# Kernel tuning notes

Measured on AMD Instinct MI355X. Metric: run time of the kernel, lower is better.

Reference implementation:

```python
import jax, jax.numpy as jnp
import numpy as np

NUM_HEADS = 16


def setup_inputs() -> dict:
    key = jax.random.key(0)
    ks = jax.random.split(key, 8)
    B, T, E = 2, 2048, 1024
    hd = E // NUM_HEADS
    return {
        "x": jax.random.normal(ks[0], (B, T, E), jnp.float32),
        "attn_mask_re": jax.random.normal(ks[1], (B, 1, T, hd // 2), jnp.float32),
        "attn_mask_im": jax.random.normal(ks[2], (B, 1, T, hd // 2), jnp.float32),
        "pad_mask": jax.random.normal(ks[3], (B, 1, 1, T), jnp.float32),
        "qkv_w": jax.random.normal(ks[4], (3 * E, E), jnp.float32) * 0.02,
        "qkv_b": jax.random.normal(ks[5], (3 * E,), jnp.float32) * 0.02,
        "o_w": jax.random.normal(ks[6], (E, E), jnp.float32) * 0.02,
        "o_b": jax.random.normal(ks[7], (E,), jnp.float32) * 0.02,
    }


def reference(x, attn_mask_re, attn_mask_im, pad_mask, qkv_w, qkv_b, o_w, o_b):
    B, T, E = x.shape
    H = NUM_HEADS
    hd = E // H
    scale = 1.0 / jnp.sqrt(jnp.asarray(hd, x.dtype))
    # fused QKV projection
    qkv = x @ qkv_w.T + qkv_b            # [B,T,3E]
    q, k, v = jnp.split(qkv, 3, axis=-1)
    q = q.reshape(B, T, H, hd).transpose(0, 2, 1, 3)          # [B,H,T,hd]
    v = v.reshape(B, T, H, hd).transpose(0, 2, 1, 3)          # [B,H,T,hd]
    # rotary on k via complex multiply: k viewed as [B,H,T,hd/2] complex
    kc = k.reshape(B, T, H, hd // 2, 2).transpose(0, 2, 1, 3, 4)  # [B,H,T,hd/2,2]
    kr, ki = kc[..., 0], kc[..., 1]
    mr, mi = attn_mask_re, attn_mask_im   # [B,1,T,hd/2] broadcast over heads
    rr = kr * mr - ki * mi
    ri = kr * mi + ki * mr
    k_rot = jnp.stack([rr, ri], axis=-1).reshape(B, H, T, hd)  # [B,H,T,hd]
    # attention scores [B,H,T,T]
    a = jnp.einsum("bhqd,bhkd->bhqk", q, k_rot) * scale
    a = a + pad_mask
    a = jax.nn.softmax(a, axis=-1)
    # (eval mode: attention dropout is a no-op)
    o = jnp.einsum("bhqk,bhkd->bhqd", a, v)                    # [B,H,T,hd]
    o = o.transpose(0, 2, 1, 3).reshape(B, T, E)
    o = o @ o_w.T + o_b
    a_avg = a.sum(axis=1) / H                                  # [B,T,T]
    return o, a_avg
```

## Files before the change

kernel.cpp:

```cpp
#include <hip/hip_runtime.h>
#include <math.h>

#define TSEQ 2048
#define EMB  1024
#define NH   16
#define HD   64
#define NB   2
#define L2E  1.4426950408889634f

#if defined(__has_builtin)
#if __has_builtin(__builtin_amdgcn_exp2f)
#define EXP2(x) __builtin_amdgcn_exp2f(x)
#else
#define EXP2(x) exp2f(x)
#endif
#else
#define EXP2(x) exp2f(x)
#endif

typedef unsigned short u16;
typedef unsigned int   u32;
typedef __attribute__((ext_vector_type(8))) short short8v;
typedef __attribute__((ext_vector_type(4))) float f32x4;

#define MFMA16(a,b,c) __builtin_amdgcn_mfma_f32_16x16x32_bf16(a,b,c,0,0,0)

__device__ inline u32 f2bf(float x) {
    u32 u = __float_as_uint(x);
    return (u + 0x7fffu + ((u >> 16) & 1u)) >> 16;
}
__device__ inline float bf2f(u32 b) { return __uint_as_float(b << 16); }
__device__ inline void split4(float x0, float x1, float x2, float x3,
                              u32& hw0, u32& hw1, u32& lw0, u32& lw1) {
    u32 h0 = f2bf(x0), h1 = f2bf(x1), h2 = f2bf(x2), h3 = f2bf(x3);
    u32 l0 = f2bf(x0 - bf2f(h0)), l1 = f2bf(x1 - bf2f(h1));
    u32 l2 = f2bf(x2 - bf2f(h2)), l3 = f2bf(x3 - bf2f(h3));
    hw0 = h0 | (h1 << 16); hw1 = h2 | (h3 << 16);
    lw0 = l0 | (l1 << 16); lw1 = l2 | (l3 << 16);
}

__global__ __launch_bounds__(256) void conv_split_kernel(
    const float* __restrict__ in, u16* __restrict__ hi, u16* __restrict__ lo)
{
    const size_t i = (size_t)blockIdx.x * 256 + threadIdx.x;
    float4 v = ((const float4*)in)[i];
    u32 hw0, hw1, lw0, lw1;
    split4(v.x, v.y, v.z, v.w, hw0, hw1, lw0, lw1);
    *(uint2*)(hi + i * 4) = make_uint2(hw0, hw1);
    *(uint2*)(lo + i * 4) = make_uint2(lw0, lw1);
}

#define MM_CORE(Ah_, Al_, Bh_, Bl_, Kdim)                                      \
    __shared__ __align__(16) u16 sAh[128][40], sAl[128][40];                   \
    __shared__ __align__(16) u16 sBh[128][40], sBl[128][40];                   \
    const int tid = threadIdx.x;                                               \
    const int lane = tid & 63, w = tid >> 6;                                   \
    const int lc = lane & 15, lg = lane >> 4;                                  \
    const int wr = w >> 1, wc = w & 1;                                         \
    const int i0 = blockIdx.x * 128, j0 = blockIdx.y * 128;                    \
    const int srow = tid >> 1, shalf = (tid & 1) << 4;                         \
    const u16* pAh = Ah_ + (size_t)(i0 + srow) * Kdim + shalf;                 \
    const u16* pAl = Al_ + (size_t)(i0 + srow) * Kdim + shalf;                 \
    const u16* pBh = Bh_ + (size_t)(j0 + srow) * Kdim + shalf;                 \
    const u16* pBl = Bl_ + (size_t)(j0 + srow) * Kdim + shalf;                 \
    f32x4 acc[4][4];                                                           \
    _Pragma("unroll")                                                          \
    for (int rs = 0; rs < 4; ++rs)                                             \
        _Pragma("unroll")                                                      \
        for (int cs = 0; cs < 4; ++cs) acc[rs][cs] = (f32x4){0.f,0.f,0.f,0.f};\
    for (int k0 = 0; k0 < Kdim; k0 += 32) {                                    \
        short8v va0 = *(const short8v*)(pAh + k0);                             \
        short8v va1 = *(const short8v*)(pAh + k0 + 8);                         \
        short8v vb0 = *(const short8v*)(pAl + k0);                             \
        short8v vb1 = *(const short8v*)(pAl + k0 + 8);                         \
        short8v vc0 = *(const short8v*)(pBh + k0);                             \
        short8v vc1 = *(const short8v*)(pBh + k0 + 8);                         \
        short8v vd0 = *(const short8v*)(pBl + k0);                             \
        short8v vd1 = *(const short8v*)(pBl + k0 + 8);                         \
        *(short8v*)&sAh[srow][shalf]     = va0;                                \
        *(short8v*)&sAh[srow][shalf + 8] = va1;                                \
        *(short8v*)&sAl[srow][shalf]     = vb0;                                \
        *(short8v*)&sAl[srow][shalf + 8] = vb1;                                \
        *(short8v*)&sBh[srow][shalf]     = vc0;                                \
        *(short8v*)&sBh[srow][shalf + 8] = vc1;                                \
        *(short8v*)&sBl[srow][shalf]     = vd0;                                \
        *(short8v*)&sBl[srow][shalf + 8] = vd1;                                \
        __syncthreads();                                                       \
        short8v fah[4], fal[4], fbh[4], fbl[4];                                \
        _Pragma("unroll")                                                      \
        for (int rs = 0; rs < 4; ++rs) {                                       \
            fah[rs] = *(const short8v*)&sAh[wr*64 + rs*16 + lc][lg*8];         \
            fal[rs] = *(const short8v*)&sAl[wr*64 + rs*16 + lc][lg*8];         \
        }                                                                      \
        _Pragma("unroll")                                                      \
        for (int cs = 0; cs < 4; ++cs) {                                       \
            fbh[cs] = *(const short8v*)&sBh[wc*64 + cs*16 + lc][lg*8];         \
            fbl[cs] = *(const short8v*)&sBl[wc*64 + cs*16 + lc][lg*8];         \
        }                                                                      \
        _Pragma("unroll")                                                      \
        for (int rs = 0; rs < 4; ++rs)                                         \
            _Pragma("unroll")                                                  \
            for (int cs = 0; cs < 4; ++cs) {                                   \
                acc[rs][cs] = MFMA16(fah[rs], fbh[cs], acc[rs][cs]);           \
                acc[rs][cs] = MFMA16(fah[rs], fbl[cs], acc[rs][cs]);           \
                acc[rs][cs] = MFMA16(fal[rs], fbh[cs], acc[rs][cs]);           \
            }                                                                  \
        __syncthreads();                                                       \
    }

__global__ __launch_bounds__(256) void mm_qkv_kernel(
    const u16* __restrict__ Ah, const u16* __restrict__ Al,
    const u16* __restrict__ Bh, const u16* __restrict__ Bl,
    const float* __restrict__ bias,
    u16* __restrict__ qhi, u16* __restrict__ qlo,
    u16* __restrict__ khi, u16* __restrict__ klo,
    u16* __restrict__ vthi, u16* __restrict__ vtlo)
{
    MM_CORE(Ah, Al, Bh, Bl, EMB)

    const int which = j0 >> 10;
    #pragma unroll
    for (int cs = 0; cs < 4; ++cs) {
        const int j = j0 + wc*64 + cs*16 + lc;
        const float bj = bias[j];
        const int e = j & (EMB - 1);
        const int hh = e >> 6, d = e & (HD - 1);
        #pragma unroll
        for (int rs = 0; rs < 4; ++rs) {
            #pragma unroll
            for (int r = 0; r < 4; ++r) {
                const int i = i0 + wr*64 + rs*16 + lg*4 + r;
                const int b = i >> 11, t = i & (TSEQ - 1);
                float val = acc[rs][cs][r] + bj;
                if (which == 0) val *= 0.125f;
                const u32 vh = f2bf(val);
                const u32 vl = f2bf(val - bf2f(vh));
                if (which == 2) {
                    const size_t ix = ((size_t)(b * NH + hh) * HD + d) * TSEQ + t;
                    vthi[ix] = (u16)vh; vtlo[ix] = (u16)vl;
                } else {
                    const size_t ix = ((size_t)(b * NH + hh) * TSEQ + t) * HD + d;
                    if (which == 0) { qhi[ix] = (u16)vh; qlo[ix] = (u16)vl; }
                    else            { khi[ix] = (u16)vh; klo[ix] = (u16)vl; }
                }
            }
        }
    }
}

__global__ __launch_bounds__(256) void mm_out_kernel(
    const u16* __restrict__ Ah, const u16* __restrict__ Al,
    const u16* __restrict__ Bh, const u16* __restrict__ Bl,
    const float* __restrict__ bias, float* __restrict__ C)
{
    MM_CORE(Ah, Al, Bh, Bl, EMB)

    #pragma unroll
    for (int cs = 0; cs < 4; ++cs) {
        const int j = j0 + wc*64 + cs*16 + lc;
        const float bj = bias[j];
        #pragma unroll
        for (int rs = 0; rs < 4; ++rs) {
            #pragma unroll
            for (int r = 0; r < 4; ++r) {
                const int i = i0 + wr*64 + rs*16 + lg*4 + r;
                C[(size_t)i * EMB + j] = acc[rs][cs][r] + bj;
            }
        }
    }
}

__global__ __launch_bounds__(256) void rotary_k_kernel(
    u16* __restrict__ khi, u16* __restrict__ klo,
    const float* __restrict__ mre, const float* __restrict__ mim)
{
    const int idx = blockIdx.x * 256 + threadIdx.x;
    const int d2 = idx & 31;
    const int t  = (idx >> 5) & (TSEQ - 1);
    const int b  = idx >> 20;
    u32 h2 = *(u32*)(khi + ((size_t)idx << 1));
    u32 l2 = *(u32*)(klo + ((size_t)idx << 1));
    float kr = bf2f(h2 & 0xffff) + bf2f(l2 & 0xffff);
    float ki = bf2f(h2 >> 16) + bf2f(l2 >> 16);
    const int mix = (b * TSEQ + t) * 32 + d2;
    const float mr = mre[mix], mi = mim[mix];
    float rr = kr * mr - ki * mi;
    float ri = kr * mi + ki * mr;
    u32 hr = f2bf(rr), hx = f2bf(ri);
    u32 lr = f2bf(rr - bf2f(hr)), lx = f2bf(ri - bf2f(hx));
    *(u32*)(khi + ((size_t)idx << 1)) = hr | (hx << 16);
    *(u32*)(klo + ((size_t)idx << 1)) = lr | (lx << 16);
}

__global__ __launch_bounds__(128) void flash_attn_kernel(
    const u16* __restrict__ qhi_, const u16* __restrict__ qlo_,
    const u16* __restrict__ khi_, const u16* __restrict__ klo_,
    const u16* __restrict__ vthi_, const u16* __restrict__ vtlo_,
    const float* __restrict__ pad,
    u16* __restrict__ ohi, u16* __restrict__ olo,
    float* __restrict__ m_out, float* __restrict__ linv_out)
{
    __shared__ __align__(16) u16 Phi[2][32*40];
    __shared__ __align__(16) u16 Plo[2][32*40];

    const int tid  = threadIdx.x;
    const int lane = tid & 63;
    const int w    = tid >> 6;
    const int bh   = blockIdx.x >> 5;
    const int sub  = blockIdx.x & 31;
    const int b    = bh >> 4, h = bh & (NH - 1);
    const int qbase = sub * 64 + w * 32;
    const int lg = lane >> 4, lc = lane & 15;

    short8v qh[2][2], ql[2][2];
    #pragma unroll
    for (int qs = 0; qs < 2; ++qs) {
        const size_t qoff = ((size_t)bh * TSEQ + qbase + qs*16 + lc) * HD + lg*8;
        #pragma unroll
        for (int s = 0; s < 2; ++s) {
            qh[qs][s] = *(const short8v*)(qhi_ + qoff + s*32);
            ql[qs][s] = *(const short8v*)(qlo_ + qoff + s*32);
        }
    }

    f32x4 O[2][4];
    float mst[2][4], lst[2][4];
    #pragma unroll
    for (int qs = 0; qs < 2; ++qs) {
        #pragma unroll
        for (int db = 0; db < 4; ++db) O[qs][db] = (f32x4){0.f,0.f,0.f,0.f};
        #pragma unroll
        for (int r = 0; r < 4; ++r) { mst[qs][r] = -1e30f; lst[qs][r] = 0.f; }
    }

    u16* PHw = &Phi[w][0];
    u16* PLw = &Plo[w][0];
    const size_t kbase  = (size_t)bh * TSEQ * HD;
    const size_t vtbase = (size_t)bh * HD * TSEQ;

    for (int k0 = 0; k0 < TSEQ; k0 += 32) {
        f32x4 S[2][2];
        #pragma unroll
        for (int qs = 0; qs < 2; ++qs)
            #pragma unroll
            for (int kb2 = 0; kb2 < 2; ++kb2) S[qs][kb2] = (f32x4){0.f,0.f,0.f,0.f};
        #pragma unroll
        for (int kb2 = 0; kb2 < 2; ++kb2) {
            #pragma unroll
            for (int s = 0; s < 2; ++s) {
                const size_t ko = kbase + (size_t)(k0 + kb2*16 + lc) * HD + s*32 + lg*8;
                short8v kh = *(const short8v*)(khi_ + ko);
                short8v kl = *(const short8v*)(klo_ + ko);
                #pragma unroll
                for (int qs = 0; qs < 2; ++qs) {
                    S[qs][kb2] = MFMA16(qh[qs][s], kh, S[qs][kb2]);
                    S[qs][kb2] = MFMA16(qh[qs][s], kl, S[qs][kb2]);
                    S[qs][kb2] = MFMA16(ql[qs][s], kh, S[qs][kb2]);
                }
            }
        }

        const float pv0 = pad[b * TSEQ + k0 + lc];
        const float pv1 = pad[b * TSEQ + k0 + 16 + lc];

        #pragma unroll
        for (int qs = 0; qs < 2; ++qs) {
            #pragma unroll
            for (int r = 0; r < 4; ++r) {
                float s0 = S[qs][0][r] + pv0;
                float s1 = S[qs][1][r] + pv1;
                float t = fmaxf(s0, s1);
                t = fmaxf(t, __shfl_xor(t, 1));
                t = fmaxf(t, __shfl_xor(t, 2));
                t = fmaxf(t, __shfl_xor(t, 4));
                t = fmaxf(t, __shfl_xor(t, 8));
                const float mn = fmaxf(mst[qs][r], t);
                const float cc = EXP2((mst[qs][r] - mn) * L2E);
                const float p0 = EXP2((s0 - mn) * L2E);
                const float p1 = EXP2((s1 - mn) * L2E);
                float ps = p0 + p1;
                ps += __shfl_xor(ps, 1);
                ps += __shfl_xor(ps, 2);
                ps += __shfl_xor(ps, 4);
                ps += __shfl_xor(ps, 8);
                lst[qs][r] = lst[qs][r] * cc + ps;
                mst[qs][r] = mn;
                const int row = qs*16 + lg*4 + r;
                const u32 h0 = f2bf(p0), h1 = f2bf(p1);
                PHw[row*40 + lc]      = (u16)h0;
                PHw[row*40 + 16 + lc] = (u16)h1;
                PLw[row*40 + lc]      = (u16)f2bf(p0 - bf2f(h0));
                PLw[row*40 + 16 + lc] = (u16)f2bf(p1 - bf2f(h1));
                #pragma unroll
                for (int db = 0; db < 4; ++db) O[qs][db][r] *= cc;
            }
        }

        short8v pfh[2], pfl[2];
        #pragma unroll
        for (int qs = 0; qs < 2; ++qs) {
            pfh[qs] = *(const short8v*)(PHw + (qs*16 + lc)*40 + lg*8);
            pfl[qs] = *(const short8v*)(PLw + (qs*16 + lc)*40 + lg*8);
        }

        #pragma unroll
        for (int db = 0; db < 4; ++db) {
            const size_t vo = vtbase + (size_t)(db*16 + lc) * TSEQ + k0 + lg*8;
            short8v vh = *(const short8v*)(vthi_ + vo);
            short8v vl = *(const short8v*)(vtlo_ + vo);
            #pragma unroll
            for (int qs = 0; qs < 2; ++qs) {
                O[qs][db] = MFMA16(pfh[qs], vh, O[qs][db]);
                O[qs][db] = MFMA16(pfh[qs], vl, O[qs][db]);
                O[qs][db] = MFMA16(pfl[qs], vh, O[qs][db]);
            }
        }
    }

    #pragma unroll
    for (int qs = 0; qs < 2; ++qs) {
        #pragma unroll
        for (int r = 0; r < 4; ++r) {
            const float inv = 1.f / lst[qs][r];
            const int trow = qbase + qs*16 + lg*4 + r;
            const size_t obase = ((size_t)(b * TSEQ + trow)) * EMB + h * HD;
            #pragma unroll
            for (int db = 0; db < 4; ++db) {
                const float val = O[qs][db][r] * inv;
                const u32 vh = f2bf(val);
                ohi[obase + db*16 + lc] = (u16)vh;
                olo[obase + db*16 + lc] = (u16)f2bf(val - bf2f(vh));
            }
            if (lc == 0) {
                m_out[bh * TSEQ + trow] = mst[qs][r];
                linv_out[bh * TSEQ + trow] = inv;
            }
        }
    }
}

__global__ __launch_bounds__(256) void attn_avg_kernel(
    const u16* __restrict__ qhi_, const u16* __restrict__ qlo_,
    const u16* __restrict__ khi_, const u16* __restrict__ klo_,
    const float* __restrict__ pad, const float* __restrict__ m_arr,
    const float* __restrict__ linv_arr, float* __restrict__ a_avg)
{
    const int tid  = threadIdx.x;
    const int lane = tid & 63;
    const int w    = tid >> 6;
    const int b  = blockIdx.z;
    const int q0 = blockIdx.y << 5;
    const int k0 = blockIdx.x << 7;
    const int lg = lane >> 4, lc = lane & 15;
    const int kw = k0 + w * 32;

    const float pv0 = pad[b * TSEQ + kw + lc];
    const float pv1 = pad[b * TSEQ + kw + 16 + lc];

    f32x4 acc[2][2];
    #pragma unroll
    for (int qs = 0; qs < 2; ++qs)
        #pragma unroll
        for (int kb2 = 0; kb2 < 2; ++kb2) acc[qs][kb2] = (f32x4){0.f,0.f,0.f,0.f};

    for (int h = 0; h < NH; ++h) {
        const size_t hb = (size_t)(b * NH + h) * TSEQ;
        short8v qh[2][2], ql[2][2];
        #pragma unroll
        for (int qs = 0; qs < 2; ++qs) {
            const size_t qoff = (hb + q0 + qs*16 + lc) * HD + lg*8;
            #pragma unroll
            for (int s = 0; s < 2; ++s) {
                qh[qs][s] = *(const short8v*)(qhi_ + qoff + s*32);
                ql[qs][s] = *(const short8v*)(qlo_ + qoff + s*32);
            }
        }
        f32x4 S[2][2];
        #pragma unroll
        for (int qs = 0; qs < 2; ++qs)
            #pragma unroll
            for (int kb2 = 0; kb2 < 2; ++kb2) S[qs][kb2] = (f32x4){0.f,0.f,0.f,0.f};
        #pragma unroll
        for (int kb2 = 0; kb2 < 2; ++kb2) {
            #pragma unroll
            for (int s = 0; s < 2; ++s) {
                const size_t ko = (hb + kw + kb2*16 + lc) * HD + s*32 + lg*8;
                short8v kh = *(const short8v*)(khi_ + ko);
                short8v kl = *(const short8v*)(klo_ + ko);
                #pragma unroll
                for (int qs = 0; qs < 2; ++qs) {
                    S[qs][kb2] = MFMA16(qh[qs][s], kh, S[qs][kb2]);
                    S[qs][kb2] = MFMA16(qh[qs][s], kl, S[qs][kb2]);
                    S[qs][kb2] = MFMA16(ql[qs][s], kh, S[qs][kb2]);
                }
            }
        }
        #pragma unroll
        for (int qs = 0; qs < 2; ++qs) {
            #pragma unroll
            for (int r = 0; r < 4; ++r) {
                const size_t rix = hb + q0 + qs*16 + lg*4 + r;
                const float mh = m_arr[rix];
                const float li = linv_arr[rix];
                acc[qs][0][r] += EXP2((S[qs][0][r] + pv0 - mh) * L2E) * li;
                acc[qs][1][r] += EXP2((S[qs][1][r] + pv1 - mh) * L2E) * li;
            }
        }
    }

    const float invH = 1.0f / (float)NH;
    #pragma unroll
    for (int qs = 0; qs < 2; ++qs) {
        #pragma unroll
        for (int r = 0; r < 4; ++r) {
            const int row = q0 + qs*16 + lg*4 + r;
            #pragma unroll
            for (int kb2 = 0; kb2 < 2; ++kb2)
                a_avg[((size_t)b * TSEQ + row) * TSEQ + kw + kb2*16 + lc] =
                    acc[qs][kb2][r] * invH;
        }
    }
}

extern "C" void kernel_launch(void* const* d_in, const int* in_sizes, int n_in,
                              void* d_out, int out_size, void* d_ws, size_t ws_size,
                              hipStream_t stream)
{
    const float* x    = (const float*)d_in[0];
    const float* mre  = (const float*)d_in[1];
    const float* mim  = (const float*)d_in[2];
    const float* pad  = (const float*)d_in[3];
    const float* qkvw = (const float*)d_in[4];
    const float* qkvb = (const float*)d_in[5];
    const float* ow   = (const float*)d_in[6];
    const float* ob   = (const float*)d_in[7];

    float* out_o = (float*)d_out;
    float* out_a = out_o + (size_t)NB * TSEQ * EMB;

    u16* ohi = (u16*)out_a;
    u16* olo = ohi + (size_t)NB * TSEQ * EMB;

    const size_t SZ = (size_t)NB * NH * TSEQ * HD;
    u16* qhi  = (u16*)d_ws;
    u16* qlo  = qhi  + SZ;
    u16* khi  = qlo  + SZ;
    u16* klo  = khi  + SZ;
    u16* vthi = klo  + SZ;
    u16* vtlo = vthi + SZ;
    float* marr = (float*)(vtlo + SZ);
    float* linv = marr + (size_t)NB * NH * TSEQ;
    u16* xhi  = (u16*)(linv + (size_t)NB * NH * TSEQ);
    u16* xlo  = xhi + SZ;
    u16* whi  = xlo + SZ;
    u16* wlo  = whi + (size_t)3 * EMB * EMB;
    u16* owhi = wlo + (size_t)3 * EMB * EMB;
    u16* owlo = owhi + (size_t)EMB * EMB;

    conv_split_kernel<<<4096, 256, 0, stream>>>(x, xhi, xlo);
    conv_split_kernel<<<3072, 256, 0, stream>>>(qkvw, whi, wlo);
    conv_split_kernel<<<1024, 256, 0, stream>>>(ow, owhi, owlo);

    mm_qkv_kernel<<<dim3(32, 24), 256, 0, stream>>>(
        xhi, xlo, whi, wlo, qkvb, qhi, qlo, khi, klo, vthi, vtlo);

    rotary_k_kernel<<<8192, 256, 0, stream>>>(khi, klo, mre, mim);

    flash_attn_kernel<<<1024, 128, 0, stream>>>(
        qhi, qlo, khi, klo, vthi, vtlo, pad, ohi, olo, marr, linv);

    mm_out_kernel<<<dim3(32, 8), 256, 0, stream>>>(
        ohi, olo, owhi, owlo, ob, out_o);

    attn_avg_kernel<<<dim3(16, 64, 2), 256, 0, stream>>>(
        qhi, qlo, khi, klo, pad, marr, linv, out_a);
}
```

Baseline: 796.1 us.

## Halve per-wave query rows in flash attention, double grid, MFMA row sums

Each wave of the flash attention kernel now handles 16 query rows instead of 32, and the grid doubles to 2048 blocks with a min-blocks launch bound of 4. This cuts register use and raises occupancy. The softmax row-sum shuffle reduction is replaced by MFMAs of the bf16 P tiles against a ones vector, and the V loads are issued before the softmax so their latency overlaps it. The cost is that each K and V tile is now loaded from global memory twice as many times overall, since fewer query rows share it, and the row sum now comes from the bf16 hi/lo split of P rather than the fp32 values.

```diff
diff --git a/kernel.cpp b/kernel.cpp
--- a/kernel.cpp
+++ b/kernel.cpp
@@ -192,7 +192,7 @@
     *(u32*)(klo + ((size_t)idx << 1)) = lr | (lx << 16);
 }
 
-__global__ __launch_bounds__(128) void flash_attn_kernel(
+__global__ __launch_bounds__(128, 4) void flash_attn_kernel(
     const u16* __restrict__ qhi_, const u16* __restrict__ qlo_,
     const u16* __restrict__ khi_, const u16* __restrict__ klo_,
     const u16* __restrict__ vthi_, const u16* __restrict__ vtlo_,
@@ -200,38 +200,36 @@
     u16* __restrict__ ohi, u16* __restrict__ olo,
     float* __restrict__ m_out, float* __restrict__ linv_out)
 {
-    __shared__ __align__(16) u16 Phi[2][32*40];
-    __shared__ __align__(16) u16 Plo[2][32*40];
+    __shared__ __align__(16) u16 Phi[2][16*40];
+    __shared__ __align__(16) u16 Plo[2][16*40];
 
     const int tid  = threadIdx.x;
     const int lane = tid & 63;
     const int w    = tid >> 6;
-    const int bh   = blockIdx.x >> 5;
-    const int sub  = blockIdx.x & 31;
+    const int bh   = blockIdx.x >> 6;
+    const int sub  = blockIdx.x & 63;
     const int b    = bh >> 4, h = bh & (NH - 1);
-    const int qbase = sub * 64 + w * 32;
+    const int qbase = sub * 32 + w * 16;
     const int lg = lane >> 4, lc = lane & 15;
 
-    short8v qh[2][2], ql[2][2];
-    #pragma unroll
-    for (int qs = 0; qs < 2; ++qs) {
-        const size_t qoff = ((size_t)bh * TSEQ + qbase + qs*16 + lc) * HD + lg*8;
-        #pragma unroll
-        for (int s = 0; s < 2; ++s) {
-            qh[qs][s] = *(const short8v*)(qhi_ + qoff + s*32);
-            ql[qs][s] = *(const short8v*)(qlo_ + qoff + s*32);
-        }
-    }
-
-    f32x4 O[2][4];
-    float mst[2][4], lst[2][4];
-    #pragma unroll
-    for (int qs = 0; qs < 2; ++qs) {
-        #pragma unroll
-        for (int db = 0; db < 4; ++db) O[qs][db] = (f32x4){0.f,0.f,0.f,0.f};
-        #pragma unroll
-        for (int r = 0; r < 4; ++r) { mst[qs][r] = -1e30f; lst[qs][r] = 0.f; }
-    }
+    short8v qh[2], ql[2];
+    {
+        const size_t qoff = ((size_t)bh * TSEQ + qbase + lc) * HD + lg*8;
+        qh[0] = *(const short8v*)(qhi_ + qoff);
+        qh[1] = *(const short8v*)(qhi_ + qoff + 32);
+        ql[0] = *(const short8v*)(qlo_ + qoff);
+        ql[1] = *(const short8v*)(qlo_ + qoff + 32);
+    }
+
+    f32x4 O[4];
+    float mst[4], lst[4];
+    #pragma unroll
+    for (int db = 0; db < 4; ++db) O[db] = (f32x4){0.f,0.f,0.f,0.f};
+    #pragma unroll
+    for (int r = 0; r < 4; ++r) { mst[r] = -1e30f; lst[r] = 0.f; }
+
+    const short oneb = (short)0x3F80;
+    const short8v ones = {oneb,oneb,oneb,oneb,oneb,oneb,oneb,oneb};
 
     u16* PHw = &Phi[w][0];
     u16* PLw = &Plo[w][0];
@@ -239,11 +237,9 @@
     const size_t vtbase = (size_t)bh * HD * TSEQ;
 
     for (int k0 = 0; k0 < TSEQ; k0 += 32) {
-        f32x4 S[2][2];
-        #pragma unroll
-        for (int qs = 0; qs < 2; ++qs)
-            #pragma unroll
-            for (int kb2 = 0; kb2 < 2; ++kb2) S[qs][kb2] = (f32x4){0.f,0.f,0.f,0.f};
+        f32x4 S[2];
+        S[0] = (f32x4){0.f,0.f,0.f,0.f};
+        S[1] = (f32x4){0.f,0.f,0.f,0.f};
         #pragma unroll
         for (int kb2 = 0; kb2 < 2; ++kb2) {
             #pragma unroll
@@ -251,90 +247,80 @@
                 const size_t ko = kbase + (size_t)(k0 + kb2*16 + lc) * HD + s*32 + lg*8;
                 short8v kh = *(const short8v*)(khi_ + ko);
                 short8v kl = *(const short8v*)(klo_ + ko);
-                #pragma unroll
-                for (int qs = 0; qs < 2; ++qs) {
-                    S[qs][kb2] = MFMA16(qh[qs][s], kh, S[qs][kb2]);
-                    S[qs][kb2] = MFMA16(qh[qs][s], kl, S[qs][kb2]);
-                    S[qs][kb2] = MFMA16(ql[qs][s], kh, S[qs][kb2]);
-                }
-            }
+                S[kb2] = MFMA16(qh[s], kh, S[kb2]);
+                S[kb2] = MFMA16(qh[s], kl, S[kb2]);
+                S[kb2] = MFMA16(ql[s], kh, S[kb2]);
+            }
+        }
+
+        short8v vh[4], vl[4];
+        #pragma unroll
+        for (int db = 0; db < 4; ++db) {
+            const size_t vo = vtbase + (size_t)(db*16 + lc) * TSEQ + k0 + lg*8;
+            vh[db] = *(const short8v*)(vthi_ + vo);
+            vl[db] = *(const short8v*)(vtlo_ + vo);
         }
 
         const float pv0 = pad[b * TSEQ + k0 + lc];
         const float pv1 = pad[b * TSEQ + k0 + 16 + lc];
 
-        #pragma unroll
-        for (int qs = 0; qs < 2; ++qs) {
-            #pragma unroll
-            for (int r = 0; r < 4; ++r) {
-                float s0 = S[qs][0][r] + pv0;
-                float s1 = S[qs][1][r] + pv1;
-                float t = fmaxf(s0, s1);
-                t = fmaxf(t, __shfl_xor(t, 1));
-                t = fmaxf(t, __shfl_xor(t, 2));
-                t = fmaxf(t, __shfl_xor(t, 4));
-                t = fmaxf(t, __shfl_xor(t, 8));
-                const float mn = fmaxf(mst[qs][r], t);
-                const float cc = EXP2((mst[qs][r] - mn) * L2E);
-                const float p0 = EXP2((s0 - mn) * L2E);
-                const float p1 = EXP2((s1 - mn) * L2E);
-                float ps = p0 + p1;
-                ps += __shfl_xor(ps, 1);
-                ps += __shfl_xor(ps, 2);
-                ps += __shfl_xor(ps, 4);
-                ps += __shfl_xor(ps, 8);
-                lst[qs][r] = lst[qs][r] * cc + ps;
-                mst[qs][r] = mn;
-                const int row = qs*16 + lg*4 + r;
-                const u32 h0 = f2bf(p0), h1 = f2bf(p1);
-                PHw[row*40 + lc]      = (u16)h0;
-                PHw[row*40 + 16 + lc] = (u16)h1;
-                PLw[row*40 + lc]      = (u16)f2bf(p0 - bf2f(h0));
-                PLw[row*40 + 16 + lc] = (u16)f2bf(p1 - bf2f(h1));
-                #pragma unroll
-                for (int db = 0; db < 4; ++db) O[qs][db][r] *= cc;
-            }
-        }
-
-        short8v pfh[2], pfl[2];
-        #pragma unroll
-        for (int qs = 0; qs < 2; ++qs) {
-            pfh[qs] = *(const short8v*)(PHw + (qs*16 + lc)*40 + lg*8);
-            pfl[qs] = *(const short8v*)(PLw + (qs*16 + lc)*40 + lg*8);
-        }
+        float cc_[4];
+        #pragma unroll
+        for (int r = 0; r < 4; ++r) {
+            float s0 = S[0][r] + pv0;
+            float s1 = S[1][r] + pv1;
+            float t = fmaxf(s0, s1);
+            t = fmaxf(t, __shfl_xor(t, 1));
+            t = fmaxf(t, __shfl_xor(t, 2));
+            t = fmaxf(t, __shfl_xor(t, 4));
+            t = fmaxf(t, __shfl_xor(t, 8));
+            const float mn = fmaxf(mst[r], t);
+            cc_[r] = EXP2((mst[r] - mn) * L2E);
+            mst[r] = mn;
+            const float p0 = EXP2((s0 - mn) * L2E);
+            const float p1 = EXP2((s1 - mn) * L2E);
+            const int row = lg*4 + r;
+            const u32 h0 = f2bf(p0), h1 = f2bf(p1);
+            PHw[row*40 + lc]      = (u16)h0;
+            PHw[row*40 + 16 + lc] = (u16)h1;
+            PLw[row*40 + lc]      = (u16)f2bf(p0 - bf2f(h0));
+            PLw[row*40 + 16 + lc] = (u16)f2bf(p1 - bf2f(h1));
+            #pragma unroll
+            for (int db = 0; db < 4; ++db) O[db][r] *= cc_[r];
+        }
+
+        short8v pfh = *(const short8v*)(PHw + lc*40 + lg*8);
+        short8v pfl = *(const short8v*)(PLw + lc*40 + lg*8);
+
+        f32x4 Ss = (f32x4){0.f,0.f,0.f,0.f};
+        Ss = MFMA16(pfh, ones, Ss);
+        Ss = MFMA16(pfl, ones, Ss);
+        #pragma unroll
+        for (int r = 0; r < 4; ++r) lst[r] = lst[r] * cc_[r] + Ss[r];
 
         #pragma unroll
         for (int db = 0; db < 4; ++db) {
-            const size_t vo = vtbase + (size_t)(db*16 + lc) * TSEQ + k0 + lg*8;
-            short8v vh = *(const short8v*)(vthi_ + vo);
-            short8v vl = *(const short8v*)(vtlo_ + vo);
-            #pragma unroll
-            for (int qs = 0; qs < 2; ++qs) {
-                O[qs][db] = MFMA16(pfh[qs], vh, O[qs][db]);
-                O[qs][db] = MFMA16(pfh[qs], vl, O[qs][db]);
-                O[qs][db] = MFMA16(pfl[qs], vh, O[qs][db]);
-            }
-        }
-    }
-
-    #pragma unroll
-    for (int qs = 0; qs < 2; ++qs) {
-        #pragma unroll
-        for (int r = 0; r < 4; ++r) {
-            const float inv = 1.f / lst[qs][r];
-            const int trow = qbase + qs*16 + lg*4 + r;
-            const size_t obase = ((size_t)(b * TSEQ + trow)) * EMB + h * HD;
-            #pragma unroll
-            for (int db = 0; db < 4; ++db) {
-                const float val = O[qs][db][r] * inv;
-                const u32 vh = f2bf(val);
-                ohi[obase + db*16 + lc] = (u16)vh;
-                olo[obase + db*16 + lc] = (u16)f2bf(val - bf2f(vh));
-            }
-            if (lc == 0) {
-                m_out[bh * TSEQ + trow] = mst[qs][r];
-                linv_out[bh * TSEQ + trow] = inv;
-            }
+            O[db] = MFMA16(pfh, vh[db], O[db]);
+            O[db] = MFMA16(pfh, vl[db], O[db]);
+            O[db] = MFMA16(pfl, vh[db], O[db]);
+        }
+    }
+
+    #pragma unroll
+    for (int r = 0; r < 4; ++r) {
+        const float inv = 1.f / lst[r];
+        const int trow = qbase + lg*4 + r;
+        const size_t obase = ((size_t)(b * TSEQ + trow)) * EMB + h * HD;
+        #pragma unroll
+        for (int db = 0; db < 4; ++db) {
+            const float val = O[db][r] * inv;
+            const u32 vhp = f2bf(val);
+            ohi[obase + db*16 + lc] = (u16)vhp;
+            olo[obase + db*16 + lc] = (u16)f2bf(val - bf2f(vhp));
+        }
+        if (lc == 0) {
+            m_out[bh * TSEQ + trow] = mst[r];
+            linv_out[bh * TSEQ + trow] = inv;
         }
     }
 }
@@ -466,7 +452,7 @@
 
     rotary_k_kernel<<<8192, 256, 0, stream>>>(khi, klo, mre, mim);
 
-    flash_attn_kernel<<<1024, 128, 0, stream>>>(
+    flash_attn_kernel<<<2048, 128, 0, stream>>>(
         qhi, qlo, khi, klo, vthi, vtlo, pad, ohi, olo, marr, linv);
 
     mm_out_kernel<<<dim3(32, 8), 256, 0, stream>>>(
```

After: 948.5 us. 1.19x slower.

## Remap blocks per XCD, prefetch V tiles, compute row sums via MFMA

Applied to the files above, without the earlier changes.

Both the flash attention and attention-average kernels now decode a linear block id so that consecutive blocks sharing the same (batch, head) or key tile land on the same XCD, which should raise L2 reuse of K/V. In flash attention, V fragments are loaded before the softmax so the load latency overlaps the exponentials. The per-row sum of probabilities now comes from an MFMA against a vector of ones instead of shuffle reductions. The MFMA row sum uses the bf16-split probabilities, so it carries a small rounding difference, and the extra live V registers may lower occupancy.

```diff
diff --git a/kernel.cpp b/kernel.cpp
--- a/kernel.cpp
+++ b/kernel.cpp
@@ -206,8 +206,11 @@
     const int tid  = threadIdx.x;
     const int lane = tid & 63;
     const int w    = tid >> 6;
-    const int bh   = blockIdx.x >> 5;
-    const int sub  = blockIdx.x & 31;
+    const int bid  = blockIdx.x;
+    const int xcd  = bid & 7;
+    const int local= bid >> 3;
+    const int bh   = xcd * 4 + (local >> 5);
+    const int sub  = local & 31;
     const int b    = bh >> 4, h = bh & (NH - 1);
     const int qbase = sub * 64 + w * 32;
     const int lg = lane >> 4, lc = lane & 15;
@@ -232,6 +235,9 @@
         #pragma unroll
         for (int r = 0; r < 4; ++r) { mst[qs][r] = -1e30f; lst[qs][r] = 0.f; }
     }
+
+    const short oneb = (short)0x3F80;
+    const short8v ones = {oneb,oneb,oneb,oneb,oneb,oneb,oneb,oneb};
 
     u16* PHw = &Phi[w][0];
     u16* PLw = &Plo[w][0];
@@ -260,9 +266,18 @@
             }
         }
 
+        short8v vh[4], vl[4];
+        #pragma unroll
+        for (int db = 0; db < 4; ++db) {
+            const size_t vo = vtbase + (size_t)(db*16 + lc) * TSEQ + k0 + lg*8;
+            vh[db] = *(const short8v*)(vthi_ + vo);
+            vl[db] = *(const short8v*)(vtlo_ + vo);
+        }
+
         const float pv0 = pad[b * TSEQ + k0 + lc];
         const float pv1 = pad[b * TSEQ + k0 + 16 + lc];
 
+        float cc_[2][4];
         #pragma unroll
         for (int qs = 0; qs < 2; ++qs) {
             #pragma unroll
@@ -275,16 +290,10 @@
                 t = fmaxf(t, __shfl_xor(t, 4));
                 t = fmaxf(t, __shfl_xor(t, 8));
                 const float mn = fmaxf(mst[qs][r], t);
-                const float cc = EXP2((mst[qs][r] - mn) * L2E);
+                cc_[qs][r] = EXP2((mst[qs][r] - mn) * L2E);
+                mst[qs][r] = mn;
                 const float p0 = EXP2((s0 - mn) * L2E);
                 const float p1 = EXP2((s1 - mn) * L2E);
-                float ps = p0 + p1;
-                ps += __shfl_xor(ps, 1);
-                ps += __shfl_xor(ps, 2);
-                ps += __shfl_xor(ps, 4);
-                ps += __shfl_xor(ps, 8);
-                lst[qs][r] = lst[qs][r] * cc + ps;
-                mst[qs][r] = mn;
                 const int row = qs*16 + lg*4 + r;
                 const u32 h0 = f2bf(p0), h1 = f2bf(p1);
                 PHw[row*40 + lc]      = (u16)h0;
@@ -292,7 +301,7 @@
                 PLw[row*40 + lc]      = (u16)f2bf(p0 - bf2f(h0));
                 PLw[row*40 + 16 + lc] = (u16)f2bf(p1 - bf2f(h1));
                 #pragma unroll
-                for (int db = 0; db < 4; ++db) O[qs][db][r] *= cc;
+                for (int db = 0; db < 4; ++db) O[qs][db][r] *= cc_[qs][r];
             }
         }
 
@@ -304,15 +313,21 @@
         }
 
         #pragma unroll
+        for (int qs = 0; qs < 2; ++qs) {
+            f32x4 Ss = (f32x4){0.f,0.f,0.f,0.f};
+            Ss = MFMA16(pfh[qs], ones, Ss);
+            Ss = MFMA16(pfl[qs], ones, Ss);
+            #pragma unroll
+            for (int r = 0; r < 4; ++r) lst[qs][r] = lst[qs][r] * cc_[qs][r] + Ss[r];
+        }
+
+        #pragma unroll
         for (int db = 0; db < 4; ++db) {
-            const size_t vo = vtbase + (size_t)(db*16 + lc) * TSEQ + k0 + lg*8;
-            short8v vh = *(const short8v*)(vthi_ + vo);
-            short8v vl = *(const short8v*)(vtlo_ + vo);
             #pragma unroll
             for (int qs = 0; qs < 2; ++qs) {
-                O[qs][db] = MFMA16(pfh[qs], vh, O[qs][db]);
-                O[qs][db] = MFMA16(pfh[qs], vl, O[qs][db]);
-                O[qs][db] = MFMA16(pfl[qs], vh, O[qs][db]);
+                O[qs][db] = MFMA16(pfh[qs], vh[db], O[qs][db]);
+                O[qs][db] = MFMA16(pfh[qs], vl[db], O[qs][db]);
+                O[qs][db] = MFMA16(pfl[qs], vh[db], O[qs][db]);
             }
         }
     }
@@ -327,9 +342,9 @@
             #pragma unroll
             for (int db = 0; db < 4; ++db) {
                 const float val = O[qs][db][r] * inv;
-                const u32 vh = f2bf(val);
-                ohi[obase + db*16 + lc] = (u16)vh;
-                olo[obase + db*16 + lc] = (u16)f2bf(val - bf2f(vh));
+                const u32 vhp = f2bf(val);
+                ohi[obase + db*16 + lc] = (u16)vhp;
+                olo[obase + db*16 + lc] = (u16)f2bf(val - bf2f(vhp));
             }
             if (lc == 0) {
                 m_out[bh * TSEQ + trow] = mst[qs][r];
@@ -348,9 +363,13 @@
     const int tid  = threadIdx.x;
     const int lane = tid & 63;
     const int w    = tid >> 6;
-    const int b  = blockIdx.z;
-    const int q0 = blockIdx.y << 5;
-    const int k0 = blockIdx.x << 7;
+    const int bid  = blockIdx.x;
+    const int xcd  = bid & 7;
+    const int local= bid >> 3;
+    const int pair = xcd * 4 + (local >> 6);
+    const int b  = pair >> 4;
+    const int k0 = (pair & 15) << 7;
+    const int q0 = (local & 63) << 5;
     const int lg = lane >> 4, lc = lane & 15;
     const int kw = k0 + w * 32;
 
@@ -472,6 +491,6 @@
     mm_out_kernel<<<dim3(32, 8), 256, 0, stream>>>(
         ohi, olo, owhi, owlo, ob, out_o);
 
-    attn_avg_kernel<<<dim3(16, 64, 2), 256, 0, stream>>>(
+    attn_avg_kernel<<<2048, 256, 0, stream>>>(
         qhi, qlo, khi, klo, pad, marr, linv, out_a);
 }
```

New measurement: 731.8 us. 8.1% less time.
